# Optimization experiments

Measured on AMD Instinct MI355X. Metric: run time of the kernel, lower is better.

The kernel has to match this reference:

```python
import jax, jax.numpy as jnp
import numpy as np

B, S, V, E, H, K = 32, 2048, 256, 512, 1024, 16


def setup_inputs() -> dict:
    key = jax.random.key(0)
    k0, k1, k2, k3, k4, k5 = jax.random.split(key, 6)
    return {
        "input_sequence": jax.random.randint(k0, (B, S), 0, V),
        "emb_table": jax.random.normal(k1, (V, E), dtype=jnp.float32),
        "conv_w": jax.random.normal(k2, (H, E, K), dtype=jnp.float32) * (1.0 / np.sqrt(E * K)),
        "conv_b": jnp.zeros((H,), dtype=jnp.float32),
        "lin_w": jax.random.normal(k4, (V, E + H), dtype=jnp.float32) * (1.0 / np.sqrt(E + H)),
        "lin_b": jnp.zeros((V,), dtype=jnp.float32),
    }


def reference(input_sequence, emb_table, conv_w, conv_b, lin_w, lin_b):
    # Embedding lookup: [B, S, E]
    emb = emb_table[input_sequence]
    # Conv1d over sequence with padding=K-1 (torch), then keep first S steps
    x = jnp.transpose(emb, (0, 2, 1))  # [B, E, S]
    y = jax.lax.conv_general_dilated(
        x, conv_w, window_strides=(1,), padding=[(K - 1, K - 1)],
        dimension_numbers=("NCH", "OIH", "NCH"))
    y = jax.nn.relu(y + conv_b[None, :, None])[:, :, :S]  # [B, H, S]
    conv_out = jnp.transpose(y, (0, 2, 1))  # [B, S, H]
    # PredNet: per-timestep cat + linear == one batched matmul over cat features
    feat = jnp.concatenate([emb, conv_out], axis=-1)  # [B, S, E+H]
    logits = jnp.einsum("bsf,vf->bsv", feat, lin_w) + lin_b
    return jax.nn.softmax(logits, axis=-1)
```

## Files before the change

### kernel.cpp

```cpp
#include <hip/hip_runtime.h>
#include <stdint.h>
#include <stddef.h>


typedef _Float16 f16;
typedef __attribute__((ext_vector_type(8))) _Float16 f16x8;
typedef __attribute__((ext_vector_type(4))) float f32x4;

#define SP 2063

__device__ __forceinline__ void gl2lds16(const void* g, void* l) {
  __builtin_amdgcn_global_load_lds((const __attribute__((address_space(1))) void*)g,
                                   (__attribute__((address_space(3))) void*)l, 16, 0, 0);
}

__global__ __launch_bounds__(256) void k_gather(const int* __restrict__ seq,
                                                const float* __restrict__ tab,
                                                f16* __restrict__ embp) {
  int row = blockIdx.x * 4 + (threadIdx.x >> 6);
  int lane = threadIdx.x & 63;
  int b = row / SP;
  int r = row - b * SP;
  f16* dst = embp + (size_t)row * 512 + lane * 8;
  if (r < 15) {
    f16x8 z = {(f16)0, (f16)0, (f16)0, (f16)0, (f16)0, (f16)0, (f16)0, (f16)0};
    *(f16x8*)dst = z;
  } else {
    int idx = seq[b * 2048 + (r - 15)];
    const float4* src = (const float4*)(tab + (size_t)idx * 512 + lane * 8);
    float4 v0 = src[0], v1 = src[1];
    f16x8 o;
    o[0] = (f16)v0.x; o[1] = (f16)v0.y; o[2] = (f16)v0.z; o[3] = (f16)v0.w;
    o[4] = (f16)v1.x; o[5] = (f16)v1.y; o[6] = (f16)v1.z; o[7] = (f16)v1.w;
    *(f16x8*)dst = o;
  }
}

__global__ __launch_bounds__(256) void k_twc(const float* __restrict__ cw,
                                             f16* __restrict__ wt2) {
  __shared__ f16 tile[8192];
  int h = blockIdx.x;
  const float4* src = (const float4*)(cw + (size_t)h * 8192);
#pragma unroll
  for (int i = 0; i < 8; ++i) {
    int o = i * 256 + threadIdx.x;
    float4 v = src[o];
    f16* d = tile + o * 4;
    d[0] = (f16)v.x; d[1] = (f16)v.y; d[2] = (f16)v.z; d[3] = (f16)v.w;
  }
  __syncthreads();
  int j = threadIdx.x >> 4, k = threadIdx.x & 15;
  f16* dst = wt2 + ((size_t)threadIdx.x * 1024 + h) * 32;
#pragma unroll
  for (int c8 = 0; c8 < 4; ++c8) {
    f16x8 v;
#pragma unroll
    for (int t = 0; t < 8; ++t) v[t] = tile[((j * 32 + c8 * 8 + t) << 4) | k];
    *(f16x8*)(dst + c8 * 8) = v;
  }
}

__global__ __launch_bounds__(256) void k_twl(const float* __restrict__ lw,
                                             f16* __restrict__ lt2) {
  int o = blockIdx.x * 256 + threadIdx.x;
  int f5 = o & 31;
  int v = (o >> 5) & 255;
  int kb = o >> 13;
  int f = (kb << 5) | f5;
  lt2[o] = (f16)lw[(size_t)v * 1536 + f];
}

__global__ __launch_bounds__(256, 3) void k_conv(const f16* __restrict__ embp,
                                                 const f16* __restrict__ wt2,
                                                 const float* __restrict__ cb,
                                                 f16* __restrict__ cout) {
  __shared__ __align__(16) f16 Asl[2 * 272 * 32];
  __shared__ __align__(16) f16 Bb[3 * 64 * 32];
  int bid = blockIdx.x;
  int x8 = bid & 7;
  int s = bid >> 3;
  int nb = s & 15;
  int mb = ((s >> 4) << 3) | x8;
  int n0 = nb << 6, m0 = mb << 8;
  int b = m0 >> 11, t0 = m0 & 2047;
  int tid = threadIdx.x, lane = tid & 63, wave = tid >> 6;
  int fr = lane & 15, q = lane >> 4;
  int prl = tid >> 2, pc = tid & 3;

  const f16* gAm[4];
#pragma unroll
  for (int c = 0; c < 4; ++c) {
    int pr = c * 64 + prl;
    int clog = pc ^ ((pr >> 1) & 3);
    gAm[c] = embp + (size_t)(b * SP + t0 + pr) * 512 + clog * 8;
  }
  const f16* gAt;
  {
    int pr = 256 + (lane >> 2);
    int clog = (lane & 3) ^ ((pr >> 1) & 3);
    gAt = embp + (size_t)(b * SP + t0 + pr) * 512 + clog * 8;
  }
  const f16* gBm;
  {
    int clog = pc ^ ((prl >> 1) & 3);
    gBm = wt2 + (size_t)(n0 + prl) * 32 + clog * 8;
  }

  int fqB = (q ^ ((fr >> 1) & 3)) << 3;

  f32x4 zero = {0.f, 0.f, 0.f, 0.f};
  f32x4 acc[4][4];
#pragma unroll
  for (int i = 0; i < 4; ++i)
#pragma unroll
    for (int jj = 0; jj < 4; ++jj) acc[i][jj] = zero;

  f16* aDst0 = Asl + wave * 512;
  f16* aTail = Asl + 8192;
  f16* bDst  = Bb + wave * 512;

#pragma unroll
  for (int c = 0; c < 4; ++c) gl2lds16(gAm[c], aDst0 + c * 2048);
  gl2lds16(gAt, aTail);
  gl2lds16(gBm, bDst);
  gl2lds16(gBm + 32768, bDst + 2048);

  int bs = 0;
#pragma unroll 1
  for (int p = 0; p < 256; ++p) {
    int t = p & 15, j = p >> 4;
    if (p == 255)               asm volatile("s_waitcnt vmcnt(0)" ::: "memory");
    else if (t == 14 && j < 15) asm volatile("s_waitcnt vmcnt(6)" ::: "memory");
    else                        asm volatile("s_waitcnt vmcnt(1)" ::: "memory");
    __builtin_amdgcn_s_barrier();
    if (p < 254) {
      int bs2 = bs + 2; if (bs2 >= 3) bs2 -= 3;
      gl2lds16(gBm + (size_t)(p + 2) * 32768, bDst + bs2 * 2048);
    }
    if (t == 13 && j < 15) {
      int abn = ((j + 1) & 1) * 8704;
#pragma unroll
      for (int c = 0; c < 4; ++c)
        gl2lds16(gAm[c] + (j + 1) * 32, aDst0 + abn + c * 2048);
      gl2lds16(gAt + (j + 1) * 32, aTail + abn);
    }
    const f16* Ab = Asl + (j & 1) * 8704;
    const f16* Bc = Bb + bs * 2048;
    f16x8 bf[4];
#pragma unroll
    for (int jj = 0; jj < 4; ++jj)
      bf[jj] = *(const f16x8*)(Bc + (jj * 16 + fr) * 32 + fqB);
    int aswz = ((t + fr) >> 1) & 3;
    const f16* ap = Ab + (size_t)(t + wave * 64 + fr) * 32 + ((q ^ aswz) << 3);
    __builtin_amdgcn_s_setprio(1);
#pragma unroll
    for (int i = 0; i < 4; ++i) {
      f16x8 af = *(const f16x8*)(ap + i * 512);
#pragma unroll
      for (int jj = 0; jj < 4; ++jj)
        acc[i][jj] = __builtin_amdgcn_mfma_f32_16x16x32_f16(af, bf[jj], acc[i][jj], 0, 0, 0);
    }
    __builtin_amdgcn_s_setprio(0);
    ++bs; if (bs == 3) bs = 0;
  }

  int col = lane & 15, rq = (lane >> 4) << 2;
  int mbase = m0 + wave * 64 + rq;
  int nbase = n0 + col;
#pragma unroll
  for (int jj = 0; jj < 4; ++jj) {
    int h = nbase + jj * 16;
    float bias = cb[h];
#pragma unroll
    for (int i = 0; i < 4; ++i) {
      int m = mbase + i * 16;
#pragma unroll
      for (int rg = 0; rg < 4; ++rg) {
        float v = acc[i][jj][rg] + bias;
        v = v > 0.f ? v : 0.f;
        cout[(size_t)(m + rg) * 1024 + h] = (f16)v;
      }
    }
  }
}

__global__ __launch_bounds__(256) void k_lin(const f16* __restrict__ embp,
                                             const f16* __restrict__ cout,
                                             const f16* __restrict__ lt2,
                                             const float* __restrict__ lb,
                                             float* __restrict__ out) {
  __shared__ __align__(16) char smem[32 * 261 * 4];
  __shared__ float pmax[4][32], psum[4][32], mrow[32], rinv[32];
  f16* As = (f16*)smem;
  f16* Bs = (f16*)(smem + 4096);
  float* Ls = (float*)smem;
  int m0 = blockIdx.x << 6;
  int b = m0 >> 11, t0 = m0 & 2047;
  int tid = threadIdx.x, lane = tid & 63, wave = tid >> 6;
  int sr = lane >> 2, sc = (lane & 3) << 3;
  const f16* gAe = embp + (size_t)(b * SP + 15 + t0 + wave * 16 + sr) * 512 + sc;
  const f16* gAc = cout + (size_t)(m0 + wave * 16 + sr) * 1024 + sc;
  f16* lA = As + wave * 512;
  int fr = lane & 15, fq = (lane >> 4) << 3;
  f32x4 zero = {0.f, 0.f, 0.f, 0.f};
  f32x4 acc[4][4];
#pragma unroll
  for (int i = 0; i < 4; ++i)
#pragma unroll
    for (int j = 0; j < 4; ++j) acc[i][j] = zero;

  for (int kb = 0; kb < 48; ++kb) {
    if (kb < 16) gl2lds16(gAe + kb * 32, lA);
    else         gl2lds16(gAc + (kb - 16) * 32, lA);
#pragma unroll
    for (int jj = 0; jj < 4; ++jj) {
      int c = wave * 4 + jj;
      gl2lds16(lt2 + (size_t)kb * 8192 + (c * 16 + sr) * 32 + sc, Bs + c * 512);
    }
    __syncthreads();
    f16x8 af[4], bf[4];
#pragma unroll
    for (int i = 0; i < 4; ++i)
      af[i] = *(const f16x8*)(As + (i * 16 + fr) * 32 + fq);
#pragma unroll
    for (int j = 0; j < 4; ++j)
      bf[j] = *(const f16x8*)(Bs + (wave * 64 + j * 16 + fr) * 32 + fq);
#pragma unroll
    for (int i = 0; i < 4; ++i)
#pragma unroll
      for (int j = 0; j < 4; ++j)
        acc[i][j] = __builtin_amdgcn_mfma_f32_16x16x32_f16(af[i], bf[j], acc[i][j], 0, 0, 0);
    __syncthreads();
  }

  int col = lane & 15, rq = (lane >> 4) << 2;
  for (int hf = 0; hf < 2; ++hf) {
    __syncthreads();
#pragma unroll
    for (int j = 0; j < 4; ++j) {
      int v = wave * 64 + j * 16 + col;
      float bias = lb[v];
#pragma unroll
      for (int i = 0; i < 2; ++i) {
        int rloc = i * 16 + rq;
        int ig = hf * 2 + i;
#pragma unroll
        for (int rg = 0; rg < 4; ++rg)
          Ls[(rloc + rg) * 261 + v] = acc[ig][j][rg] + bias;
      }
    }
    __syncthreads();
    if (tid < 128) {
      int r = tid & 31, qd = tid >> 5;
      const float* rowp = Ls + r * 261 + qd * 64;
      float pm = -1e30f;
#pragma unroll 8
      for (int c = 0; c < 64; ++c) pm = fmaxf(pm, rowp[c]);
      pmax[qd][r] = pm;
    }
    __syncthreads();
    if (tid < 32)
      mrow[tid] = fmaxf(fmaxf(pmax[0][tid], pmax[1][tid]), fmaxf(pmax[2][tid], pmax[3][tid]));
    __syncthreads();
    if (tid < 128) {
      int r = tid & 31, qd = tid >> 5;
      const float* rowp = Ls + r * 261 + qd * 64;
      float mr = mrow[r], ps = 0.f;
#pragma unroll 8
      for (int c = 0; c < 64; ++c) ps += __expf(rowp[c] - mr);
      psum[qd][r] = ps;
    }
    __syncthreads();
    if (tid < 32)
      rinv[tid] = 1.f / (psum[0][tid] + psum[1][tid] + psum[2][tid] + psum[3][tid]);
    __syncthreads();
    float* obase = out + (size_t)(m0 + hf * 32) * 256 + tid;
#pragma unroll 4
    for (int r = 0; r < 32; ++r)
      obase[(size_t)r * 256] = __expf(Ls[r * 261 + tid] - mrow[r]) * rinv[r];
  }
}

extern "C" void kernel_launch(void* const* d_in, const int* in_sizes, int n_in,
                              void* d_out, int out_size, void* d_ws, size_t ws_size,
                              hipStream_t stream) {
  const int*   seq = (const int*)d_in[0];
  const float* tab = (const float*)d_in[1];
  const float* cw  = (const float*)d_in[2];
  const float* cb  = (const float*)d_in[3];
  const float* lw  = (const float*)d_in[4];
  const float* lb  = (const float*)d_in[5];
  float* out = (float*)d_out;
  char* ws = (char*)d_ws;
  f16* embp = (f16*)(ws);
  f16* cout = (f16*)(ws + 67600384);
  f16* wt2  = (f16*)(ws + 201818112);
  f16* lt2  = (f16*)(ws + 218595328);

  hipLaunchKernelGGL(k_gather, dim3(16504), dim3(256), 0, stream, seq, tab, embp);
  hipLaunchKernelGGL(k_twc,    dim3(1024),  dim3(256), 0, stream, cw, wt2);
  hipLaunchKernelGGL(k_twl,    dim3(1536),  dim3(256), 0, stream, lw, lt2);
  hipLaunchKernelGGL(k_conv,   dim3(4096),  dim3(256), 0, stream, embp, wt2, cb, cout);
  hipLaunchKernelGGL(k_lin,    dim3(1024),  dim3(256), 0, stream, embp, cout, lt2, lb, out);
}
```

Before: 1.154 ms.

## Restructure conv pipeline into 4-tap groups with double-buffered weights and single A buffer

The conv main loop now processes four kernel taps per iteration, using a double-buffered weight tile that holds four taps. This replaces the per-tap triple-buffered scheme with fine-grained vmcnt waits. The A (embedding) tile drops to a single buffer that is reloaded synchronously between channel chunks, and the raw barriers become __syncthreads. The aim is fewer barriers per MFMA, but the A reload is no longer overlapped with compute, so it stalls, and the relaxed waits may expose more load latency.

```diff
diff --git a/kernel.cpp b/kernel.cpp
--- a/kernel.cpp
+++ b/kernel.cpp
@@ -74,8 +74,8 @@
                                                  const f16* __restrict__ wt2,
                                                  const float* __restrict__ cb,
                                                  f16* __restrict__ cout) {
-  __shared__ __align__(16) f16 Asl[2 * 272 * 32];
-  __shared__ __align__(16) f16 Bb[3 * 64 * 32];
+  __shared__ __align__(16) f16 Asl[272 * 32];
+  __shared__ __align__(16) f16 Bb[2 * 4 * 64 * 32];
   int bid = blockIdx.x;
   int x8 = bid & 7;
   int s = bid >> 3;
@@ -115,53 +115,50 @@
 #pragma unroll
     for (int jj = 0; jj < 4; ++jj) acc[i][jj] = zero;
 
-  f16* aDst0 = Asl + wave * 512;
-  f16* aTail = Asl + 8192;
-  f16* bDst  = Bb + wave * 512;
-
-#pragma unroll
-  for (int c = 0; c < 4; ++c) gl2lds16(gAm[c], aDst0 + c * 2048);
-  gl2lds16(gAt, aTail);
-  gl2lds16(gBm, bDst);
-  gl2lds16(gBm + 32768, bDst + 2048);
-
-  int bs = 0;
+  f16* aD0 = Asl + wave * 512;
+  f16* bD0 = Bb + wave * 512;
+
+#pragma unroll
+  for (int c = 0; c < 4; ++c) gl2lds16(gAm[c], aD0 + c * 2048);
+  gl2lds16(gAt, Asl + 8192);
+#pragma unroll
+  for (int t = 0; t < 4; ++t) gl2lds16(gBm + (size_t)t * 32768, bD0 + t * 2048);
+  __syncthreads();
+
 #pragma unroll 1
-  for (int p = 0; p < 256; ++p) {
-    int t = p & 15, j = p >> 4;
-    if (p == 255)               asm volatile("s_waitcnt vmcnt(0)" ::: "memory");
-    else if (t == 14 && j < 15) asm volatile("s_waitcnt vmcnt(6)" ::: "memory");
-    else                        asm volatile("s_waitcnt vmcnt(1)" ::: "memory");
-    __builtin_amdgcn_s_barrier();
-    if (p < 254) {
-      int bs2 = bs + 2; if (bs2 >= 3) bs2 -= 3;
-      gl2lds16(gBm + (size_t)(p + 2) * 32768, bDst + bs2 * 2048);
-    }
-    if (t == 13 && j < 15) {
-      int abn = ((j + 1) & 1) * 8704;
-#pragma unroll
-      for (int c = 0; c < 4; ++c)
-        gl2lds16(gAm[c] + (j + 1) * 32, aDst0 + abn + c * 2048);
-      gl2lds16(gAt + (j + 1) * 32, aTail + abn);
-    }
-    const f16* Ab = Asl + (j & 1) * 8704;
-    const f16* Bc = Bb + bs * 2048;
-    f16x8 bf[4];
-#pragma unroll
-    for (int jj = 0; jj < 4; ++jj)
-      bf[jj] = *(const f16x8*)(Bc + (jj * 16 + fr) * 32 + fqB);
-    int aswz = ((t + fr) >> 1) & 3;
-    const f16* ap = Ab + (size_t)(t + wave * 64 + fr) * 32 + ((q ^ aswz) << 3);
-    __builtin_amdgcn_s_setprio(1);
-#pragma unroll
-    for (int i = 0; i < 4; ++i) {
-      f16x8 af = *(const f16x8*)(ap + i * 512);
+  for (int g = 0; g < 64; ++g) {
+    int j = g >> 2;
+    if (g < 63) {
+      const f16* src = gBm + (size_t)(g + 1) * 4 * 32768;
+      f16* dst = bD0 + ((g + 1) & 1) * 8192;
+#pragma unroll
+      for (int t = 0; t < 4; ++t) gl2lds16(src + (size_t)t * 32768, dst + t * 2048);
+    }
+    const f16* Bc = Bb + (g & 1) * 8192;
+#pragma unroll
+    for (int t = 0; t < 4; ++t) {
+      int k = ((g & 3) << 2) + t;
+      int aswz = ((k + fr) >> 1) & 3;
+      const f16* ap = Asl + (size_t)(k + wave * 64 + fr) * 32 + ((q ^ aswz) << 3);
+      f16x8 bf[4];
 #pragma unroll
       for (int jj = 0; jj < 4; ++jj)
-        acc[i][jj] = __builtin_amdgcn_mfma_f32_16x16x32_f16(af, bf[jj], acc[i][jj], 0, 0, 0);
-    }
-    __builtin_amdgcn_s_setprio(0);
-    ++bs; if (bs == 3) bs = 0;
+        bf[jj] = *(const f16x8*)(Bc + t * 2048 + (jj * 16 + fr) * 32 + fqB);
+#pragma unroll
+      for (int i = 0; i < 4; ++i) {
+        f16x8 af = *(const f16x8*)(ap + i * 512);
+#pragma unroll
+        for (int jj = 0; jj < 4; ++jj)
+          acc[i][jj] = __builtin_amdgcn_mfma_f32_16x16x32_f16(af, bf[jj], acc[i][jj], 0, 0, 0);
+      }
+    }
+    __syncthreads();
+    if ((g & 3) == 3 && j < 15) {
+#pragma unroll
+      for (int c = 0; c < 4; ++c) gl2lds16(gAm[c] + (j + 1) * 32, aD0 + c * 2048);
+      gl2lds16(gAt + (j + 1) * 32, Asl + 8192);
+      __syncthreads();
+    }
   }
 
   int col = lane & 15, rq = (lane >> 4) << 2;
```

Result: faster. 1.034 ms (-10.4%).
